# Kernel optimization log

Measured on AMD Instinct MI355X. Metric: run time of the kernel, lower is better.

The kernel has to match this reference:

```python
import jax, jax.numpy as jnp
import numpy as np

MI, MH, MO = 8, 16, 8  # multiplicities of (0e,1o) in in/hidden/out irreps
NB = 262144

_eps = np.zeros((3, 3, 3), dtype=np.float32)
_eps[0, 1, 2] = _eps[1, 2, 0] = _eps[2, 0, 1] = 1.0
_eps[0, 2, 1] = _eps[2, 1, 0] = _eps[1, 0, 2] = -1.0
EPS_LC = jnp.asarray(_eps)  # Levi-Civita; w3j(1,1,1) = eps/sqrt(6)


def fctp(s, v, w_ss, w_vv0, w_sv, w_vs, w_vv1):
    """FullyConnectedTensorProduct for irreps (ms x 0e + mv x 1o) -> (mw x 0e + mw_v x 1o).
    e3nn 'component' irrep normalization + 'element' path normalization:
    path_weight = sqrt(ir_out.dim / sum_paths(mul1*mul2)).
    w3j(0,0,0)=1, w3j(1,1,0)=delta/sqrt(3), w3j(0,1,1)=delta/sqrt(3), w3j(1,1,1)=eps/sqrt(6)."""
    ms, mv = s.shape[1], v.shape[1]
    c0 = (1.0 / (ms * ms + mv * mv)) ** 0.5          # scalar output: paths ss->s, vv->s
    c1 = (3.0 / (2 * ms * mv + mv * mv)) ** 0.5      # vector output: paths sv, vs, vv
    inv3 = 3.0 ** -0.5
    inv6 = 6.0 ** -0.5
    out_s = c0 * (jnp.einsum('bu,bv,uvw->bw', s, s, w_ss)
                  + inv3 * jnp.einsum('bui,bvi,uvw->bw', v, v, w_vv0))
    out_v = c1 * (inv3 * (jnp.einsum('bu,bvi,uvw->bwi', s, v, w_sv)
                          + jnp.einsum('bui,bv,uvw->bwi', v, s, w_vs))
                  + inv6 * jnp.einsum('bui,bvj,uvw,ijk->bwk', v, v, w_vv1, EPS_LC))
    return out_s, out_v


def si_norm(ys, yv, eps=1e-9):
    """SelfInteraction variance normalization (torch.std is unbiased -> ddof=1)."""
    std_s = jnp.std(ys, axis=1, ddof=1)
    ys = ys / (std_s[:, None] + eps)
    norm1 = jnp.sqrt(jnp.sum(yv ** 2, axis=2) + eps)   # [nb, mv]
    std_v = jnp.std(norm1, axis=1, ddof=1)
    yv = yv / (std_v[:, None, None] + eps)
    return ys, yv


def tv_norm(xs, xv, eps=1e-6):
    xs = xs / jnp.sqrt(jnp.sum(xs ** 2, axis=1, keepdims=True) + eps)
    # faithful to torch: sum over channel dim -> [nb,3], then mean over the 3 comps
    norm1 = jnp.sqrt(jnp.sum(xv ** 2, axis=1) + eps)   # [nb, 3]
    norm_mean = jnp.mean(norm1, axis=1)                # [nb]
    xv = xv / (norm_mean[:, None, None] + eps)
    return xs, xv


def setup_inputs() -> dict:
    key = jax.random.key(0)
    ks = jax.random.split(key, 11)
    x = jax.random.normal(ks[0], (NB, MI + 3 * MI), dtype=jnp.float32)
    # e3nn initializes tensor-product weights ~ N(0,1); normalization via path weights
    w1 = {n: jax.random.normal(k, (MI, MI, MH), dtype=jnp.float32)
          for n, k in zip(['w1_ss', 'w1_vv0', 'w1_sv', 'w1_vs', 'w1_vv1'], ks[1:6])}
    w2 = {n: jax.random.normal(k, (MH, MH, MO), dtype=jnp.float32)
          for n, k in zip(['w2_ss', 'w2_vv0', 'w2_sv', 'w2_vs', 'w2_vv1'], ks[6:11])}
    return {'x': x, **w1, **w2}


def reference(x, w1_ss, w1_vv0, w1_sv, w1_vs, w1_vv1,
              w2_ss, w2_vv0, w2_sv, w2_vs, w2_vv1):
    nb = x.shape[0]
    # layout: [scalars(MI) | vectors(MI*3, u-major)]
    xs = jnp.tanh(x[:, :MI])                    # Activation(tanh) on l=0 only
    xv = x[:, MI:].reshape(nb, MI, 3)
    ys, yv = fctp(xs, xv, w1_ss, w1_vv0, w1_sv, w1_vs, w1_vv1)   # si1 tensor product
    ys, yv = si_norm(ys, yv)                    # si1 variance normalization
    ys, yv = tv_norm(ys, yv)                    # TvNorm
    zs, zv = fctp(ys, yv, w2_ss, w2_vv0, w2_sv, w2_vs, w2_vv1)   # si2 tensor product
    zs, zv = si_norm(zs, zv)
    zs = jax.nn.sigmoid(zs)                     # Activation(sigmoid) on l=0 only
    return jnp.concatenate([zs, zv.reshape(nb, MO * 3)], axis=1)
```

## Files before the change

kernel.cpp:

```cpp
#include <hip/hip_runtime.h>
#include <math.h>

#define NBROWS 262144

typedef float v2f __attribute__((ext_vector_type(2)));
__device__ __forceinline__ v2f sp(float x){ v2f r; r.x = x; r.y = x; return r; }

#define WS_TOT 7808

__device__ void pair_le(int p, int M, int& u, int& v) {
    u = 0; int cnt = M;
    while (p >= cnt) { p -= cnt; ++u; cnt = M - u; }
    v = u + p;
}
__device__ void pair_lt(int p, int M, int& u, int& v) {
    u = 0; int cnt = M - 1;
    while (p >= cnt) { p -= cnt; ++u; cnt = M - 1 - u; }
    v = u + 1 + p;
}

__global__ __launch_bounds__(256) void prep_kernel(
    const float* __restrict__ w1_ss, const float* __restrict__ w1_vv0,
    const float* __restrict__ w1_sv, const float* __restrict__ w1_vs,
    const float* __restrict__ w1_vv1,
    const float* __restrict__ w2_ss, const float* __restrict__ w2_vv0,
    const float* __restrict__ w2_sv, const float* __restrict__ w2_vs,
    const float* __restrict__ w2_vv1,
    float* __restrict__ ws)
{
    const float inv3 = 0.5773502691896258f;
    const float inv6 = 0.4082482904638631f;
    int i = blockIdx.x * 256 + threadIdx.x;
    if (i >= WS_TOT) return;
    float val = 0.f;
    if (i < 1152) {
        int p = i >> 5, r = i & 31;
        int which = r >> 4, w = r & 15;
        int u, v; pair_le(p, 8, u, v);
        const float c0 = 0.08838834764831845f;
        const float* src = which ? w1_vv0 : w1_ss;
        float cc = which ? c0 * inv3 : c0;
        val = (u == v) ? cc * src[(u*8+v)*16+w]
                       : cc * (src[(u*8+v)*16+w] + src[(v*8+u)*16+w]);
    } else if (i < 2176) {
        int r = i - 1152; int vv = r >> 7, rem = r & 127, u = rem >> 4, w = rem & 15;
        val = (0.125f * inv3) * (w1_sv[(u*8+vv)*16+w] + w1_vs[(vv*8+u)*16+w]);
    } else if (i < 2624) {
        int r = i - 2176; int p = r >> 4, w = r & 15;
        int u, v; pair_lt(p, 8, u, v);
        val = (0.125f * inv6) * (w1_vv1[(u*8+v)*16+w] - w1_vv1[(v*8+u)*16+w]);
    } else if (i < 4800) {
        int r = i - 2624; int p = r >> 4, rr = r & 15, which = rr >> 3, w = rr & 7;
        int u, v; pair_le(p, 16, u, v);
        const float c0 = 0.04419417382415922f;
        const float* src = which ? w2_vv0 : w2_ss;
        float cc = which ? c0 * inv3 : c0;
        val = (u == v) ? cc * src[(u*16+v)*8+w]
                       : cc * (src[(u*16+v)*8+w] + src[(v*16+u)*8+w]);
    } else if (i < 6848) {
        int r = i - 4800; int vv = r >> 7, rem = r & 127, u = rem >> 3, w = rem & 7;
        val = (0.0625f * inv3) * (w2_sv[(u*16+vv)*8+w] + w2_vs[(vv*16+u)*8+w]);
    } else {
        int r = i - 6848; int p = r >> 3, w = r & 7;
        int u, v; pair_lt(p, 16, u, v);
        val = (0.0625f * inv6) * (w2_vv1[(u*16+v)*8+w] - w2_vv1[(v*16+u)*8+w]);
    }
    ws[i] = val;
}

template<int W0>
__device__ __forceinline__ void l1_chunk(const float* Wl,
    const float (&s)[8], const float (&v)[8][3],
    v2f (&ys2)[8], v2f (&ox)[8], v2f (&oy)[8], v2f (&oz)[8])
{
    const int J0 = W0 / 2;
#pragma unroll
    for (int j = 0; j < 4; ++j) { ys2[J0+j]=sp(0.f); ox[J0+j]=sp(0.f); oy[J0+j]=sp(0.f); oz[J0+j]=sp(0.f); }
    {
        int p = 0;
#pragma unroll
        for (int u = 0; u < 8; ++u)
#pragma unroll
        for (int vv = u; vv < 8; ++vv) {
            float pp = s[u] * s[vv];
            float dd = v[u][0]*v[vv][0] + v[u][1]*v[vv][1] + v[u][2]*v[vv][2];
            const v2f* qa = reinterpret_cast<const v2f*>(Wl + p*32 + W0);
            const v2f* qb = reinterpret_cast<const v2f*>(Wl + p*32 + 16 + W0);
            v2f vp = sp(pp), vd = sp(dd);
#pragma unroll
            for (int j = 0; j < 4; ++j) ys2[J0+j] += vp*qa[j] + vd*qb[j];
            ++p;
        }
    }
#pragma unroll
    for (int vv = 0; vv < 8; ++vv) {
        v2f tw[4];
#pragma unroll
        for (int j = 0; j < 4; ++j) tw[j] = sp(0.f);
#pragma unroll
        for (int u = 0; u < 8; ++u) {
            const v2f* qc = reinterpret_cast<const v2f*>(Wl + 1152 + (vv*8+u)*16 + W0);
            v2f su = sp(s[u]);
#pragma unroll
            for (int j = 0; j < 4; ++j) tw[j] += su*qc[j];
        }
        v2f vx = sp(v[vv][0]), vy = sp(v[vv][1]), vz = sp(v[vv][2]);
#pragma unroll
        for (int j = 0; j < 4; ++j) {
            ox[J0+j] += tw[j]*vx; oy[J0+j] += tw[j]*vy; oz[J0+j] += tw[j]*vz;
        }
    }
    {
        int p = 0;
#pragma unroll
        for (int u = 0; u < 8; ++u)
#pragma unroll
        for (int vv = u + 1; vv < 8; ++vv) {
            float cx = v[u][1]*v[vv][2] - v[u][2]*v[vv][1];
            float cy = v[u][2]*v[vv][0] - v[u][0]*v[vv][2];
            float cz = v[u][0]*v[vv][1] - v[u][1]*v[vv][0];
            const v2f* qa = reinterpret_cast<const v2f*>(Wl + 2176 + p*16 + W0);
            v2f vcx = sp(cx), vcy = sp(cy), vcz = sp(cz);
#pragma unroll
            for (int j = 0; j < 4; ++j) {
                v2f a = qa[j];
                ox[J0+j] += vcx*a; oy[J0+j] += vcy*a; oz[J0+j] += vcz*a;
            }
            ++p;
        }
    }
}

__device__ __forceinline__ void l2_pass(const float* Wl,
    const float (&s)[16], const float (&v)[16][3],
    v2f (&zs2)[4], v2f (&zx)[4], v2f (&zy)[4], v2f (&zz)[4])
{
#pragma unroll
    for (int j = 0; j < 4; ++j) { zs2[j]=sp(0.f); zx[j]=sp(0.f); zy[j]=sp(0.f); zz[j]=sp(0.f); }
    {
        int p = 0;
#pragma unroll
        for (int u = 0; u < 16; ++u)
#pragma unroll
        for (int vv = u; vv < 16; ++vv) {
            float pp = s[u] * s[vv];
            float dd = v[u][0]*v[vv][0] + v[u][1]*v[vv][1] + v[u][2]*v[vv][2];
            const v2f* qa = reinterpret_cast<const v2f*>(Wl + 2624 + p*16);
            const v2f* qb = reinterpret_cast<const v2f*>(Wl + 2624 + p*16 + 8);
            v2f vp = sp(pp), vd = sp(dd);
#pragma unroll
            for (int j = 0; j < 4; ++j) zs2[j] += vp*qa[j] + vd*qb[j];
            ++p;
        }
    }
#pragma unroll
    for (int vv = 0; vv < 16; ++vv) {
        v2f tw[4];
#pragma unroll
        for (int j = 0; j < 4; ++j) tw[j] = sp(0.f);
#pragma unroll
        for (int u = 0; u < 16; ++u) {
            const v2f* qc = reinterpret_cast<const v2f*>(Wl + 4800 + (vv*16+u)*8);
            v2f su = sp(s[u]);
#pragma unroll
            for (int j = 0; j < 4; ++j) tw[j] += su*qc[j];
        }
        v2f vx = sp(v[vv][0]), vy = sp(v[vv][1]), vz = sp(v[vv][2]);
#pragma unroll
        for (int j = 0; j < 4; ++j) {
            zx[j] += tw[j]*vx; zy[j] += tw[j]*vy; zz[j] += tw[j]*vz;
        }
    }
    {
        int p = 0;
#pragma unroll
        for (int u = 0; u < 16; ++u)
#pragma unroll
        for (int vv = u + 1; vv < 16; ++vv) {
            float cx = v[u][1]*v[vv][2] - v[u][2]*v[vv][1];
            float cy = v[u][2]*v[vv][0] - v[u][0]*v[vv][2];
            float cz = v[u][0]*v[vv][1] - v[u][1]*v[vv][0];
            const v2f* qa = reinterpret_cast<const v2f*>(Wl + 6848 + p*8);
            v2f vcx = sp(cx), vcy = sp(cy), vcz = sp(cz);
#pragma unroll
            for (int j = 0; j < 4; ++j) {
                v2f a = qa[j];
                zx[j] += vcx*a; zy[j] += vcy*a; zz[j] += vcz*a;
            }
            ++p;
        }
    }
}

__device__ __forceinline__ void si_norm16_v(v2f (&ys2)[8], v2f (&ox)[8], v2f (&oy)[8], v2f (&oz)[8])
{
    v2f a = sp(0.f);
#pragma unroll
    for (int j = 0; j < 8; ++j) a += ys2[j];
    float m = (a.x + a.y) * (1.f/16);
    v2f vr = sp(0.f);
#pragma unroll
    for (int j = 0; j < 8; ++j) { v2f d = ys2[j] - sp(m); vr += d*d; }
    float inv = 1.f / (sqrtf((vr.x+vr.y) * (1.f/15)) + 1e-9f);
#pragma unroll
    for (int j = 0; j < 8; ++j) ys2[j] *= sp(inv);

    float n1[16]; float sum = 0.f;
#pragma unroll
    for (int j = 0; j < 8; ++j) {
        v2f nn = ox[j]*ox[j] + oy[j]*oy[j] + oz[j]*oz[j];
        n1[2*j]   = sqrtf(nn.x + 1e-9f);
        n1[2*j+1] = sqrtf(nn.y + 1e-9f);
        sum += n1[2*j] + n1[2*j+1];
    }
    float mn = sum * (1.f/16);
    float var = 0.f;
#pragma unroll
    for (int i = 0; i < 16; ++i) { float d = n1[i] - mn; var += d*d; }
    float invv = 1.f / (sqrtf(var * (1.f/15)) + 1e-9f);
    v2f vi = sp(invv);
#pragma unroll
    for (int j = 0; j < 8; ++j) { ox[j] *= vi; oy[j] *= vi; oz[j] *= vi; }
}

__device__ __forceinline__ void tv_norm16_v(v2f (&ys2)[8], v2f (&ox)[8], v2f (&oy)[8], v2f (&oz)[8])
{
    v2f ssum = sp(0.f);
#pragma unroll
    for (int j = 0; j < 8; ++j) ssum += ys2[j]*ys2[j];
    float inv = 1.f / sqrtf(ssum.x + ssum.y + 1e-6f);
#pragma unroll
    for (int j = 0; j < 8; ++j) ys2[j] *= sp(inv);

    v2f sx = sp(0.f), sy = sp(0.f), sz = sp(0.f);
#pragma unroll
    for (int j = 0; j < 8; ++j) { sx += ox[j]*ox[j]; sy += oy[j]*oy[j]; sz += oz[j]*oz[j]; }
    float nm = (sqrtf(sx.x+sx.y+1e-6f) + sqrtf(sy.x+sy.y+1e-6f) + sqrtf(sz.x+sz.y+1e-6f)) * (1.f/3.f);
    float invv = 1.f / (nm + 1e-6f);
#pragma unroll
    for (int j = 0; j < 8; ++j) { ox[j] *= sp(invv); oy[j] *= sp(invv); oz[j] *= sp(invv); }
}

__device__ __forceinline__ void si_norm8_v(v2f (&zs2)[4], v2f (&zx)[4], v2f (&zy)[4], v2f (&zz)[4])
{
    v2f a = sp(0.f);
#pragma unroll
    for (int j = 0; j < 4; ++j) a += zs2[j];
    float m = (a.x + a.y) * (1.f/8);
    v2f vr = sp(0.f);
#pragma unroll
    for (int j = 0; j < 4; ++j) { v2f d = zs2[j] - sp(m); vr += d*d; }
    float inv = 1.f / (sqrtf((vr.x+vr.y) * (1.f/7)) + 1e-9f);
#pragma unroll
    for (int j = 0; j < 4; ++j) zs2[j] *= sp(inv);

    float n1[8]; float sum = 0.f;
#pragma unroll
    for (int j = 0; j < 4; ++j) {
        v2f nn = zx[j]*zx[j] + zy[j]*zy[j] + zz[j]*zz[j];
        n1[2*j]   = sqrtf(nn.x + 1e-9f);
        n1[2*j+1] = sqrtf(nn.y + 1e-9f);
        sum += n1[2*j] + n1[2*j+1];
    }
    float mn = sum * (1.f/8);
    float var = 0.f;
#pragma unroll
    for (int i = 0; i < 8; ++i) { float d = n1[i] - mn; var += d*d; }
    float invv = 1.f / (sqrtf(var * (1.f/7)) + 1e-9f);
    v2f vi = sp(invv);
#pragma unroll
    for (int j = 0; j < 4; ++j) { zx[j] *= vi; zy[j] *= vi; zz[j] *= vi; }
}

__device__ __forceinline__ float fast_tanh(float x) {
    return 1.f - 2.f / (__expf(2.f * x) + 1.f);
}

__global__ __launch_bounds__(256) void DoubleLayer_main_kernel(
    const float* __restrict__ x,
    const float* __restrict__ ws,
    float* __restrict__ out)
{
    __shared__ float Wl[WS_TOT];

    int row = blockIdx.x * 256 + threadIdx.x;
    const float4* xr = reinterpret_cast<const float4*>(x + (size_t)row * 32);
    float4 q0 = xr[0], q1 = xr[1], q2 = xr[2], q3 = xr[3];
    float4 q4 = xr[4], q5 = xr[5], q6 = xr[6], q7 = xr[7];

#pragma unroll
    for (int i = 0; i < 8; ++i) {
        int idx = threadIdx.x + i * 256;
        if (idx < WS_TOT/4)
            reinterpret_cast<float4*>(Wl)[idx] = reinterpret_cast<const float4*>(ws)[idx];
    }
    __syncthreads();

    float s1[8];
    s1[0] = fast_tanh(q0.x); s1[1] = fast_tanh(q0.y); s1[2] = fast_tanh(q0.z); s1[3] = fast_tanh(q0.w);
    s1[4] = fast_tanh(q1.x); s1[5] = fast_tanh(q1.y); s1[6] = fast_tanh(q1.z); s1[7] = fast_tanh(q1.w);
    float v1[8][3];
    v1[0][0]=q2.x; v1[0][1]=q2.y; v1[0][2]=q2.z;
    v1[1][0]=q2.w; v1[1][1]=q3.x; v1[1][2]=q3.y;
    v1[2][0]=q3.z; v1[2][1]=q3.w; v1[2][2]=q4.x;
    v1[3][0]=q4.y; v1[3][1]=q4.z; v1[3][2]=q4.w;
    v1[4][0]=q5.x; v1[4][1]=q5.y; v1[4][2]=q5.z;
    v1[5][0]=q5.w; v1[5][1]=q6.x; v1[5][2]=q6.y;
    v1[6][0]=q6.z; v1[6][1]=q6.w; v1[6][2]=q7.x;
    v1[7][0]=q7.y; v1[7][1]=q7.z; v1[7][2]=q7.w;

    v2f ys2[8], ox[8], oy[8], oz[8];
    l1_chunk<0>(Wl, s1, v1, ys2, ox, oy, oz);
    __builtin_amdgcn_sched_barrier(0);
    l1_chunk<8>(Wl, s1, v1, ys2, ox, oy, oz);
    __builtin_amdgcn_sched_barrier(0);

    si_norm16_v(ys2, ox, oy, oz);
    tv_norm16_v(ys2, ox, oy, oz);
    __builtin_amdgcn_sched_barrier(0);

    float s2[16], vv2[16][3];
#pragma unroll
    for (int j = 0; j < 8; ++j) {
        s2[2*j] = ys2[j].x;   s2[2*j+1] = ys2[j].y;
        vv2[2*j][0] = ox[j].x; vv2[2*j+1][0] = ox[j].y;
        vv2[2*j][1] = oy[j].x; vv2[2*j+1][1] = oy[j].y;
        vv2[2*j][2] = oz[j].x; vv2[2*j+1][2] = oz[j].y;
    }

    v2f zs2[4], zx[4], zy[4], zz[4];
    l2_pass(Wl, s2, vv2, zs2, zx, zy, zz);
    __builtin_amdgcn_sched_barrier(0);

    si_norm8_v(zs2, zx, zy, zz);

    float o[32];
#pragma unroll
    for (int j = 0; j < 4; ++j) {
        o[2*j]   = 1.f / (1.f + __expf(-zs2[j].x));
        o[2*j+1] = 1.f / (1.f + __expf(-zs2[j].y));
    }
#pragma unroll
    for (int j = 0; j < 4; ++j) {
        int w0 = 2*j, w1 = 2*j+1;
        o[8+3*w0+0] = zx[j].x; o[8+3*w0+1] = zy[j].x; o[8+3*w0+2] = zz[j].x;
        o[8+3*w1+0] = zx[j].y; o[8+3*w1+1] = zy[j].y; o[8+3*w1+2] = zz[j].y;
    }
    float4* orow = reinterpret_cast<float4*>(out + (size_t)row * 32);
#pragma unroll
    for (int i = 0; i < 8; ++i) orow[i] = make_float4(o[4*i+0], o[4*i+1], o[4*i+2], o[4*i+3]);
}

extern "C" void kernel_launch(void* const* d_in, const int* in_sizes, int n_in,
                              void* d_out, int out_size, void* d_ws, size_t ws_size,
                              hipStream_t stream)
{
    const float* x = (const float*)d_in[0];
    float* ws = (float*)d_ws;
    prep_kernel<<<31, 256, 0, stream>>>(
        (const float*)d_in[1], (const float*)d_in[2], (const float*)d_in[3],
        (const float*)d_in[4], (const float*)d_in[5],
        (const float*)d_in[6], (const float*)d_in[7], (const float*)d_in[8],
        (const float*)d_in[9], (const float*)d_in[10], ws);
    DoubleLayer_main_kernel<<<NBROWS/256, 256, 0, stream>>>(x, ws, (float*)d_out);
}
```

Baseline: 202.9 us.

## Move packed weights from LDS to constant memory and use scalar FMAs

Precomputed weights now live in a __constant__ array, filled by a device-to-device copy to the symbol after the prep kernel. The main kernel drops the per-block LDS staging and the __syncthreads. All weight accesses are uniform across the wavefront, so they can become scalar loads feeding SGPR operands. The packed v2f math is also replaced by plain scalar float FMAs, which gives up packed-FMA throughput and adds a memcpy to the launch sequence.

After: 437.0 us. +115.4%, slower.

```diff
diff --git a/kernel.cpp b/kernel.cpp
--- a/kernel.cpp
+++ b/kernel.cpp
@@ -2,18 +2,17 @@
 #include <math.h>
 
 #define NBROWS 262144
-
-typedef float v2f __attribute__((ext_vector_type(2)));
-__device__ __forceinline__ v2f sp(float x){ v2f r; r.x = x; r.y = x; return r; }
-
 #define WS_TOT 7808
 
-__device__ void pair_le(int p, int M, int& u, int& v) {
+__constant__ float cw[WS_TOT];
+
+
+__device__ __forceinline__ void pair_le(int p, int M, int& u, int& v) {
     u = 0; int cnt = M;
     while (p >= cnt) { p -= cnt; ++u; cnt = M - u; }
     v = u + p;
 }
-__device__ void pair_lt(int p, int M, int& u, int& v) {
+__device__ __forceinline__ void pair_lt(int p, int M, int& u, int& v) {
     u = 0; int cnt = M - 1;
     while (p >= cnt) { p -= cnt; ++u; cnt = M - 1 - u; }
     v = u + 1 + p;
@@ -69,13 +68,12 @@
 }
 
 template<int W0>
-__device__ __forceinline__ void l1_chunk(const float* Wl,
+__device__ __forceinline__ void l1_chunk(
     const float (&s)[8], const float (&v)[8][3],
-    v2f (&ys2)[8], v2f (&ox)[8], v2f (&oy)[8], v2f (&oz)[8])
-{
-    const int J0 = W0 / 2;
-#pragma unroll
-    for (int j = 0; j < 4; ++j) { ys2[J0+j]=sp(0.f); ox[J0+j]=sp(0.f); oy[J0+j]=sp(0.f); oz[J0+j]=sp(0.f); }
+    float (&ys)[16], float (&ox)[16], float (&oy)[16], float (&oz)[16])
+{
+#pragma unroll
+    for (int w = 0; w < 8; ++w) { ys[W0+w]=0.f; ox[W0+w]=0.f; oy[W0+w]=0.f; oz[W0+w]=0.f; }
     {
         int p = 0;
 #pragma unroll
@@ -84,30 +82,28 @@
         for (int vv = u; vv < 8; ++vv) {
             float pp = s[u] * s[vv];
             float dd = v[u][0]*v[vv][0] + v[u][1]*v[vv][1] + v[u][2]*v[vv][2];
-            const v2f* qa = reinterpret_cast<const v2f*>(Wl + p*32 + W0);
-            const v2f* qb = reinterpret_cast<const v2f*>(Wl + p*32 + 16 + W0);
-            v2f vp = sp(pp), vd = sp(dd);
-#pragma unroll
-            for (int j = 0; j < 4; ++j) ys2[J0+j] += vp*qa[j] + vd*qb[j];
+#pragma unroll
+            for (int w = 0; w < 8; ++w)
+                ys[W0+w] += pp * cw[p*32 + W0 + w] + dd * cw[p*32 + 16 + W0 + w];
             ++p;
         }
     }
 #pragma unroll
     for (int vv = 0; vv < 8; ++vv) {
-        v2f tw[4];
-#pragma unroll
-        for (int j = 0; j < 4; ++j) tw[j] = sp(0.f);
+        float tw[8];
+#pragma unroll
+        for (int w = 0; w < 8; ++w) tw[w] = 0.f;
 #pragma unroll
         for (int u = 0; u < 8; ++u) {
-            const v2f* qc = reinterpret_cast<const v2f*>(Wl + 1152 + (vv*8+u)*16 + W0);
-            v2f su = sp(s[u]);
-#pragma unroll
-            for (int j = 0; j < 4; ++j) tw[j] += su*qc[j];
-        }
-        v2f vx = sp(v[vv][0]), vy = sp(v[vv][1]), vz = sp(v[vv][2]);
-#pragma unroll
-        for (int j = 0; j < 4; ++j) {
-            ox[J0+j] += tw[j]*vx; oy[J0+j] += tw[j]*vy; oz[J0+j] += tw[j]*vz;
+            float su = s[u];
+#pragma unroll
+            for (int w = 0; w < 8; ++w) tw[w] += su * cw[1152 + (vv*8+u)*16 + W0 + w];
+        }
+#pragma unroll
+        for (int w = 0; w < 8; ++w) {
+            ox[W0+w] += tw[w] * v[vv][0];
+            oy[W0+w] += tw[w] * v[vv][1];
+            oz[W0+w] += tw[w] * v[vv][2];
         }
     }
     {
@@ -119,24 +115,22 @@
             float cx = v[u][1]*v[vv][2] - v[u][2]*v[vv][1];
             float cy = v[u][2]*v[vv][0] - v[u][0]*v[vv][2];
             float cz = v[u][0]*v[vv][1] - v[u][1]*v[vv][0];
-            const v2f* qa = reinterpret_cast<const v2f*>(Wl + 2176 + p*16 + W0);
-            v2f vcx = sp(cx), vcy = sp(cy), vcz = sp(cz);
-#pragma unroll
-            for (int j = 0; j < 4; ++j) {
-                v2f a = qa[j];
-                ox[J0+j] += vcx*a; oy[J0+j] += vcy*a; oz[J0+j] += vcz*a;
+#pragma unroll
+            for (int w = 0; w < 8; ++w) {
+                float a = cw[2176 + p*16 + W0 + w];
+                ox[W0+w] += a*cx; oy[W0+w] += a*cy; oz[W0+w] += a*cz;
             }
             ++p;
         }
     }
 }
 
-__device__ __forceinline__ void l2_pass(const float* Wl,
-    const float (&s)[16], const float (&v)[16][3],
-    v2f (&zs2)[4], v2f (&zx)[4], v2f (&zy)[4], v2f (&zz)[4])
-{
-#pragma unroll
-    for (int j = 0; j < 4; ++j) { zs2[j]=sp(0.f); zx[j]=sp(0.f); zy[j]=sp(0.f); zz[j]=sp(0.f); }
+__device__ __forceinline__ void l2_pass(
+    const float (&s)[16], const float (&vx)[16], const float (&vy)[16], const float (&vz)[16],
+    float (&zs)[8], float (&zx)[8], float (&zy)[8], float (&zz)[8])
+{
+#pragma unroll
+    for (int w = 0; w < 8; ++w) { zs[w]=0.f; zx[w]=0.f; zy[w]=0.f; zz[w]=0.f; }
     {
         int p = 0;
 #pragma unroll
@@ -144,31 +138,29 @@
 #pragma unroll
         for (int vv = u; vv < 16; ++vv) {
             float pp = s[u] * s[vv];
-            float dd = v[u][0]*v[vv][0] + v[u][1]*v[vv][1] + v[u][2]*v[vv][2];
-            const v2f* qa = reinterpret_cast<const v2f*>(Wl + 2624 + p*16);
-            const v2f* qb = reinterpret_cast<const v2f*>(Wl + 2624 + p*16 + 8);
-            v2f vp = sp(pp), vd = sp(dd);
-#pragma unroll
-            for (int j = 0; j < 4; ++j) zs2[j] += vp*qa[j] + vd*qb[j];
+            float dd = vx[u]*vx[vv] + vy[u]*vy[vv] + vz[u]*vz[vv];
+#pragma unroll
+            for (int w = 0; w < 8; ++w)
+                zs[w] += pp * cw[2624 + p*16 + w] + dd * cw[2624 + p*16 + 8 + w];
             ++p;
         }
     }
 #pragma unroll
     for (int vv = 0; vv < 16; ++vv) {
-        v2f tw[4];
-#pragma unroll
-        for (int j = 0; j < 4; ++j) tw[j] = sp(0.f);
+        float tw[8];
+#pragma unroll
+        for (int w = 0; w < 8; ++w) tw[w] = 0.f;
 #pragma unroll
         for (int u = 0; u < 16; ++u) {
-            const v2f* qc = reinterpret_cast<const v2f*>(Wl + 4800 + (vv*16+u)*8);
-            v2f su = sp(s[u]);
-#pragma unroll
-            for (int j = 0; j < 4; ++j) tw[j] += su*qc[j];
-        }
-        v2f vx = sp(v[vv][0]), vy = sp(v[vv][1]), vz = sp(v[vv][2]);
-#pragma unroll
-        for (int j = 0; j < 4; ++j) {
-            zx[j] += tw[j]*vx; zy[j] += tw[j]*vy; zz[j] += tw[j]*vz;
+            float su = s[u];
+#pragma unroll
+            for (int w = 0; w < 8; ++w) tw[w] += su * cw[4800 + (vv*16+u)*8 + w];
+        }
+#pragma unroll
+        for (int w = 0; w < 8; ++w) {
+            zx[w] += tw[w] * vx[vv];
+            zy[w] += tw[w] * vy[vv];
+            zz[w] += tw[w] * vz[vv];
         }
     }
     {
@@ -177,99 +169,91 @@
         for (int u = 0; u < 16; ++u)
 #pragma unroll
         for (int vv = u + 1; vv < 16; ++vv) {
-            float cx = v[u][1]*v[vv][2] - v[u][2]*v[vv][1];
-            float cy = v[u][2]*v[vv][0] - v[u][0]*v[vv][2];
-            float cz = v[u][0]*v[vv][1] - v[u][1]*v[vv][0];
-            const v2f* qa = reinterpret_cast<const v2f*>(Wl + 6848 + p*8);
-            v2f vcx = sp(cx), vcy = sp(cy), vcz = sp(cz);
-#pragma unroll
-            for (int j = 0; j < 4; ++j) {
-                v2f a = qa[j];
-                zx[j] += vcx*a; zy[j] += vcy*a; zz[j] += vcz*a;
+            float cx = vy[u]*vz[vv] - vz[u]*vy[vv];
+            float cy = vz[u]*vx[vv] - vx[u]*vz[vv];
+            float cz = vx[u]*vy[vv] - vy[u]*vx[vv];
+#pragma unroll
+            for (int w = 0; w < 8; ++w) {
+                float a = cw[6848 + p*8 + w];
+                zx[w] += a*cx; zy[w] += a*cy; zz[w] += a*cz;
             }
             ++p;
         }
     }
 }
 
-__device__ __forceinline__ void si_norm16_v(v2f (&ys2)[8], v2f (&ox)[8], v2f (&oy)[8], v2f (&oz)[8])
-{
-    v2f a = sp(0.f);
-#pragma unroll
-    for (int j = 0; j < 8; ++j) a += ys2[j];
-    float m = (a.x + a.y) * (1.f/16);
-    v2f vr = sp(0.f);
-#pragma unroll
-    for (int j = 0; j < 8; ++j) { v2f d = ys2[j] - sp(m); vr += d*d; }
-    float inv = 1.f / (sqrtf((vr.x+vr.y) * (1.f/15)) + 1e-9f);
-#pragma unroll
-    for (int j = 0; j < 8; ++j) ys2[j] *= sp(inv);
-
-    float n1[16]; float sum = 0.f;
-#pragma unroll
-    for (int j = 0; j < 8; ++j) {
-        v2f nn = ox[j]*ox[j] + oy[j]*oy[j] + oz[j]*oz[j];
-        n1[2*j]   = sqrtf(nn.x + 1e-9f);
-        n1[2*j+1] = sqrtf(nn.y + 1e-9f);
-        sum += n1[2*j] + n1[2*j+1];
-    }
-    float mn = sum * (1.f/16);
+__device__ __forceinline__ void si_norm16_s(float (&ys)[16], float (&ox)[16], float (&oy)[16], float (&oz)[16])
+{
+    float sum = 0.f;
+#pragma unroll
+    for (int i = 0; i < 16; ++i) sum += ys[i];
+    float m = sum * (1.f/16);
     float var = 0.f;
 #pragma unroll
-    for (int i = 0; i < 16; ++i) { float d = n1[i] - mn; var += d*d; }
-    float invv = 1.f / (sqrtf(var * (1.f/15)) + 1e-9f);
-    v2f vi = sp(invv);
-#pragma unroll
-    for (int j = 0; j < 8; ++j) { ox[j] *= vi; oy[j] *= vi; oz[j] *= vi; }
-}
-
-__device__ __forceinline__ void tv_norm16_v(v2f (&ys2)[8], v2f (&ox)[8], v2f (&oy)[8], v2f (&oz)[8])
-{
-    v2f ssum = sp(0.f);
-#pragma unroll
-    for (int j = 0; j < 8; ++j) ssum += ys2[j]*ys2[j];
-    float inv = 1.f / sqrtf(ssum.x + ssum.y + 1e-6f);
-#pragma unroll
-    for (int j = 0; j < 8; ++j) ys2[j] *= sp(inv);
-
-    v2f sx = sp(0.f), sy = sp(0.f), sz = sp(0.f);
-#pragma unroll
-    for (int j = 0; j < 8; ++j) { sx += ox[j]*ox[j]; sy += oy[j]*oy[j]; sz += oz[j]*oz[j]; }
-    float nm = (sqrtf(sx.x+sx.y+1e-6f) + sqrtf(sy.x+sy.y+1e-6f) + sqrtf(sz.x+sz.y+1e-6f)) * (1.f/3.f);
+    for (int i = 0; i < 16; ++i) { float d = ys[i] - m; var += d*d; }
+    float inv = 1.f / (sqrtf(var * (1.f/15)) + 1e-9f);
+#pragma unroll
+    for (int i = 0; i < 16; ++i) ys[i] *= inv;
+
+    float n1[16]; float sn = 0.f;
+#pragma unroll
+    for (int i = 0; i < 16; ++i) {
+        n1[i] = sqrtf(ox[i]*ox[i] + oy[i]*oy[i] + oz[i]*oz[i] + 1e-9f);
+        sn += n1[i];
+    }
+    float mn = sn * (1.f/16);
+    float vr = 0.f;
+#pragma unroll
+    for (int i = 0; i < 16; ++i) { float d = n1[i] - mn; vr += d*d; }
+    float invv = 1.f / (sqrtf(vr * (1.f/15)) + 1e-9f);
+#pragma unroll
+    for (int i = 0; i < 16; ++i) { ox[i] *= invv; oy[i] *= invv; oz[i] *= invv; }
+}
+
+__device__ __forceinline__ void tv_norm16_s(float (&ys)[16], float (&ox)[16], float (&oy)[16], float (&oz)[16])
+{
+    float ss = 0.f;
+#pragma unroll
+    for (int i = 0; i < 16; ++i) ss += ys[i]*ys[i];
+    float inv = 1.f / sqrtf(ss + 1e-6f);
+#pragma unroll
+    for (int i = 0; i < 16; ++i) ys[i] *= inv;
+
+    float a0 = 0.f, a1 = 0.f, a2 = 0.f;
+#pragma unroll
+    for (int i = 0; i < 16; ++i) { a0 += ox[i]*ox[i]; a1 += oy[i]*oy[i]; a2 += oz[i]*oz[i]; }
+    float nm = (sqrtf(a0+1e-6f) + sqrtf(a1+1e-6f) + sqrtf(a2+1e-6f)) * (1.f/3.f);
     float invv = 1.f / (nm + 1e-6f);
 #pragma unroll
-    for (int j = 0; j < 8; ++j) { ox[j] *= sp(invv); oy[j] *= sp(invv); oz[j] *= sp(invv); }
-}
-
-__device__ __forceinline__ void si_norm8_v(v2f (&zs2)[4], v2f (&zx)[4], v2f (&zy)[4], v2f (&zz)[4])
-{
-    v2f a = sp(0.f);
-#pragma unroll
-    for (int j = 0; j < 4; ++j) a += zs2[j];
-    float m = (a.x + a.y) * (1.f/8);
-    v2f vr = sp(0.f);
-#pragma unroll
-    for (int j = 0; j < 4; ++j) { v2f d = zs2[j] - sp(m); vr += d*d; }
-    float inv = 1.f / (sqrtf((vr.x+vr.y) * (1.f/7)) + 1e-9f);
-#pragma unroll
-    for (int j = 0; j < 4; ++j) zs2[j] *= sp(inv);
-
-    float n1[8]; float sum = 0.f;
-#pragma unroll
-    for (int j = 0; j < 4; ++j) {
-        v2f nn = zx[j]*zx[j] + zy[j]*zy[j] + zz[j]*zz[j];
-        n1[2*j]   = sqrtf(nn.x + 1e-9f);
-        n1[2*j+1] = sqrtf(nn.y + 1e-9f);
-        sum += n1[2*j] + n1[2*j+1];
-    }
-    float mn = sum * (1.f/8);
+    for (int i = 0; i < 16; ++i) { ox[i] *= invv; oy[i] *= invv; oz[i] *= invv; }
+}
+
+__device__ __forceinline__ void si_norm8_s(float (&zs)[8], float (&zx)[8], float (&zy)[8], float (&zz)[8])
+{
+    float sum = 0.f;
+#pragma unroll
+    for (int i = 0; i < 8; ++i) sum += zs[i];
+    float m = sum * (1.f/8);
     float var = 0.f;
 #pragma unroll
-    for (int i = 0; i < 8; ++i) { float d = n1[i] - mn; var += d*d; }
-    float invv = 1.f / (sqrtf(var * (1.f/7)) + 1e-9f);
-    v2f vi = sp(invv);
-#pragma unroll
-    for (int j = 0; j < 4; ++j) { zx[j] *= vi; zy[j] *= vi; zz[j] *= vi; }
+    for (int i = 0; i < 8; ++i) { float d = zs[i] - m; var += d*d; }
+    float inv = 1.f / (sqrtf(var * (1.f/7)) + 1e-9f);
+#pragma unroll
+    for (int i = 0; i < 8; ++i) zs[i] *= inv;
+
+    float n1[8]; float sn = 0.f;
+#pragma unroll
+    for (int i = 0; i < 8; ++i) {
+        n1[i] = sqrtf(zx[i]*zx[i] + zy[i]*zy[i] + zz[i]*zz[i] + 1e-9f);
+        sn += n1[i];
+    }
+    float mn = sn * (1.f/8);
+    float vr = 0.f;
+#pragma unroll
+    for (int i = 0; i < 8; ++i) { float d = n1[i] - mn; vr += d*d; }
+    float invv = 1.f / (sqrtf(vr * (1.f/7)) + 1e-9f);
+#pragma unroll
+    for (int i = 0; i < 8; ++i) { zx[i] *= invv; zy[i] *= invv; zz[i] *= invv; }
 }
 
 __device__ __forceinline__ float fast_tanh(float x) {
@@ -278,23 +262,12 @@
 
 __global__ __launch_bounds__(256) void DoubleLayer_main_kernel(
     const float* __restrict__ x,
-    const float* __restrict__ ws,
     float* __restrict__ out)
 {
-    __shared__ float Wl[WS_TOT];
-
     int row = blockIdx.x * 256 + threadIdx.x;
     const float4* xr = reinterpret_cast<const float4*>(x + (size_t)row * 32);
     float4 q0 = xr[0], q1 = xr[1], q2 = xr[2], q3 = xr[3];
     float4 q4 = xr[4], q5 = xr[5], q6 = xr[6], q7 = xr[7];
-
-#pragma unroll
-    for (int i = 0; i < 8; ++i) {
-        int idx = threadIdx.x + i * 256;
-        if (idx < WS_TOT/4)
-            reinterpret_cast<float4*>(Wl)[idx] = reinterpret_cast<const float4*>(ws)[idx];
-    }
-    __syncthreads();
 
     float s1[8];
     s1[0] = fast_tanh(q0.x); s1[1] = fast_tanh(q0.y); s1[2] = fast_tanh(q0.z); s1[3] = fast_tanh(q0.w);
@@ -309,42 +282,28 @@
     v1[6][0]=q6.z; v1[6][1]=q6.w; v1[6][2]=q7.x;
     v1[7][0]=q7.y; v1[7][1]=q7.z; v1[7][2]=q7.w;
 
-    v2f ys2[8], ox[8], oy[8], oz[8];
-    l1_chunk<0>(Wl, s1, v1, ys2, ox, oy, oz);
+    float ys[16], ox[16], oy[16], oz[16];
+    l1_chunk<0>(s1, v1, ys, ox, oy, oz);
     __builtin_amdgcn_sched_barrier(0);
-    l1_chunk<8>(Wl, s1, v1, ys2, ox, oy, oz);
+    l1_chunk<8>(s1, v1, ys, ox, oy, oz);
     __builtin_amdgcn_sched_barrier(0);
 
-    si_norm16_v(ys2, ox, oy, oz);
-    tv_norm16_v(ys2, ox, oy, oz);
+    si_norm16_s(ys, ox, oy, oz);
+    tv_norm16_s(ys, ox, oy, oz);
     __builtin_amdgcn_sched_barrier(0);
 
-    float s2[16], vv2[16][3];
-#pragma unroll
-    for (int j = 0; j < 8; ++j) {
-        s2[2*j] = ys2[j].x;   s2[2*j+1] = ys2[j].y;
-        vv2[2*j][0] = ox[j].x; vv2[2*j+1][0] = ox[j].y;
-        vv2[2*j][1] = oy[j].x; vv2[2*j+1][1] = oy[j].y;
-        vv2[2*j][2] = oz[j].x; vv2[2*j+1][2] = oz[j].y;
-    }
-
-    v2f zs2[4], zx[4], zy[4], zz[4];
-    l2_pass(Wl, s2, vv2, zs2, zx, zy, zz);
+    float zs[8], zx[8], zy[8], zz[8];
+    l2_pass(ys, ox, oy, oz, zs, zx, zy, zz);
     __builtin_amdgcn_sched_barrier(0);
 
-    si_norm8_v(zs2, zx, zy, zz);
+    si_norm8_s(zs, zx, zy, zz);
 
     float o[32];
 #pragma unroll
-    for (int j = 0; j < 4; ++j) {
-        o[2*j]   = 1.f / (1.f + __expf(-zs2[j].x));
-        o[2*j+1] = 1.f / (1.f + __expf(-zs2[j].y));
-    }
-#pragma unroll
-    for (int j = 0; j < 4; ++j) {
-        int w0 = 2*j, w1 = 2*j+1;
-        o[8+3*w0+0] = zx[j].x; o[8+3*w0+1] = zy[j].x; o[8+3*w0+2] = zz[j].x;
-        o[8+3*w1+0] = zx[j].y; o[8+3*w1+1] = zy[j].y; o[8+3*w1+2] = zz[j].y;
+    for (int w = 0; w < 8; ++w) o[w] = 1.f / (1.f + __expf(-zs[w]));
+#pragma unroll
+    for (int w = 0; w < 8; ++w) {
+        o[8+3*w+0] = zx[w]; o[8+3*w+1] = zy[w]; o[8+3*w+2] = zz[w];
     }
     float4* orow = reinterpret_cast<float4*>(out + (size_t)row * 32);
 #pragma unroll
@@ -362,5 +321,7 @@
         (const float*)d_in[4], (const float*)d_in[5],
         (const float*)d_in[6], (const float*)d_in[7], (const float*)d_in[8],
         (const float*)d_in[9], (const float*)d_in[10], ws);
-    DoubleLayer_main_kernel<<<NBROWS/256, 256, 0, stream>>>(x, ws, (float*)d_out);
-}
+    hipMemcpyToSymbolAsync(HIP_SYMBOL(cw), ws, WS_TOT * sizeof(float), 0,
+                           hipMemcpyDeviceToDevice, stream);
+    DoubleLayer_main_kernel<<<NBROWS/256, 256, 0, stream>>>(x, (float*)d_out);
+}
```
